# Kernel optimization log

Measured on AMD Instinct MI355X. Metric: run time of the kernel, lower is better.

Reference implementation:

```python
import jax, jax.numpy as jnp
import numpy as np

S = 16   # num_states
C = 8    # input_channels
B = 64   # batch
L = 4096 # sequence length


def hyperbolic_sigmoid(x):
    return x / (1 + jnp.abs(x)) * 0.5 + 0.5


def hyperbolic_softmax(logits, axis):
    x = hyperbolic_sigmoid(logits)
    return x / jnp.sum(x, axis=axis, keepdims=True)


def setup_inputs() -> dict:
    key = jax.random.key(0)
    k0, k1, k2, k3 = jax.random.split(key, 4)
    return {
        "log_input_probs": jax.random.normal(k0, (B, L, C), dtype=jnp.float32),
        "invh_initial_state_probs": jax.random.normal(k1, (S,), dtype=jnp.float32),
        "invh_transition_probs": jax.random.normal(k2, (S, C, S), dtype=jnp.float32),
        "invh_accepting_state_probs": jax.random.normal(k3, (S,), dtype=jnp.float32),
    }


def reference(log_input_probs, invh_initial_state_probs, invh_transition_probs, invh_accepting_state_probs):
    # hyperbolic parameterization -> probabilities
    initial_state_probs = hyperbolic_softmax(invh_initial_state_probs, axis=0)         # (S,)
    transition_probs = hyperbolic_softmax(invh_transition_probs, axis=2)               # (S,C,S)
    accepting_state_logprobs = jnp.log(hyperbolic_sigmoid(invh_accepting_state_probs)) # (S,)

    input_probs = jnp.exp(log_input_probs)  # (B,L,C)
    # per-timestep transition matrices, (B,L,S,S)
    trans_each = jnp.einsum('pcn,blc->blpn', transition_probs, input_probs)
    # log-depth chain product m0 @ m1 @ ... @ m_{L-1} via associative scan
    prefix = jax.lax.associative_scan(jnp.matmul, trans_each, axis=1)
    transition_overall = prefix[:, -1]  # (B,S,S)
    # p_state[b,n] = sum_p overall[b,p,n] * init[p]
    p_state = jnp.einsum('bpn,p->bn', transition_overall, initial_state_probs)
    log_p_state = jnp.log(p_state + 1e-20)
    log_acceptance = jax.nn.logsumexp(log_p_state + accepting_state_logprobs[None, :], axis=1)  # (B,)
    return log_acceptance[None]  # (1,B)
```

## Files before the change

### kernel.cpp

```cpp
#include <hip/hip_runtime.h>
#include <hip/hip_bf16.h>
#include <math.h>

#define S 16
#define C 8
#define NB 64
#define L 4096
#define K 64
#define LC 64

#define SLOT 324
#define RS 20
#define XSS 10

typedef __attribute__((ext_vector_type(8))) short bf16x8;
typedef __attribute__((ext_vector_type(4))) short bf16x4;
typedef __attribute__((ext_vector_type(4))) float f32x4;
typedef unsigned long long ull;

#define WS_INIT 0
#define WS_ACC  64
#define WS_CLOG 512
#define WS_TTT  16896
#define WS_CP   49664

__device__ __forceinline__ float hsig(float x) {
    return x / (1.0f + fabsf(x)) * 0.5f + 0.5f;
}
__device__ __forceinline__ unsigned int f2bf2(float a, float b) {
    __hip_bfloat162 h = __float22bfloat162_rn(make_float2(a, b));
    unsigned int u; __builtin_memcpy(&u, &h, 4); return u;
}
__device__ __forceinline__ unsigned short f2bf(float f) {
    __hip_bfloat16 h = __float2bfloat16(f);
    unsigned short u; __builtin_memcpy(&u, &h, 2); return u;
}

__device__ __forceinline__ f32x4 mfma16(bf16x4 a, bf16x4 b, f32x4 c) {
#if __has_builtin(__builtin_amdgcn_mfma_f32_16x16x16bf16_1k)
    return __builtin_amdgcn_mfma_f32_16x16x16bf16_1k(a, b, c, 0, 0, 0);
#else
    bf16x8 a8 = {a[0], a[1], a[2], a[3], 0, 0, 0, 0};
    bf16x8 b8 = {b[0], b[1], b[2], b[3], 0, 0, 0, 0};
    return __builtin_amdgcn_mfma_f32_16x16x32_bf16(a8, b8, c, 0, 0, 0);
#endif
}

__device__ __forceinline__ bf16x4 ldfrag4(const unsigned short* base, int lane) {
    return *(const bf16x4*)(base + (lane & 15) * RS + (lane >> 4) * 4);
}
__device__ __forceinline__ bf16x4 ldfrag_g4(const unsigned short* base, int lane) {
    return *(const bf16x4*)(base + (lane & 15) * 16 + (lane >> 4) * 4);
}
__device__ __forceinline__ bf16x4 cvt4(f32x4 d) {
    union { unsigned int u[2]; bf16x4 v; } cv;
    cv.u[0] = f2bf2(d[0], d[1]);
    cv.u[1] = f2bf2(d[2], d[3]);
    return cv.v;
}
__device__ __forceinline__ void store16(unsigned short* slot, f32x4 d, int lane, bool odd) {
    int col = lane & 15, quad = lane >> 4;
    if (odd) {
        ull pk = (ull)f2bf2(d[0], d[1]) | ((ull)f2bf2(d[2], d[3]) << 32);
        *(ull*)(slot + col * RS + quad * 4) = pk;
    } else {
#pragma unroll
        for (int r = 0; r < 4; r++) slot[(quad * 4 + r) * RS + col] = f2bf(d[r]);
    }
}

__device__ __forceinline__ f32x4 tree_upper(unsigned short* slots, int lane, int w,
                                            bf16x4 B1a, bf16x4 B1b) {
    f32x4 z = {0.f, 0.f, 0.f, 0.f};
    f32x4 dA = mfma16(ldfrag4(slots + (8 * w) * SLOT, lane), B1a, z);
    store16(slots + (8 * w) * SLOT, dA, lane, false);
    f32x4 dB = mfma16(ldfrag4(slots + (8 * w + 4) * SLOT, lane), B1b, z);
    bf16x4 B2 = cvt4(dB);
    f32x4 d3 = mfma16(ldfrag4(slots + (8 * w) * SLOT, lane), B2, z);
    store16(slots + (8 * w) * SLOT, d3, lane, w & 1);
    __syncthreads();
    if (w < 2) {
        f32x4 d4 = mfma16(ldfrag4(slots + (16 * w) * SLOT, lane),
                          ldfrag4(slots + (16 * w + 8) * SLOT, lane), z);
        store16(slots + (16 * w) * SLOT, d4, lane, w & 1);
    }
    __syncthreads();
    return mfma16(ldfrag4(slots, lane), ldfrag4(slots + 16 * SLOT, lane), z);
}

__global__ void __launch_bounds__(256) prepall_kernel(const float* __restrict__ invh_init,
                                                      const float* __restrict__ invh_T,
                                                      const float* __restrict__ invh_acc,
                                                      unsigned char* __restrict__ wsb) {
    __shared__ float Tn[2048];
    int t = threadIdx.x;
    int cc = blockIdx.x, c = cc >> 3, c2 = cc & 7;
    if (t < S * C) {
        float v[S]; float s = 0.f;
#pragma unroll
        for (int n = 0; n < S; n++) { v[n] = hsig(invh_T[t * S + n]); s += v[n]; }
        float inv = 1.f / s;
#pragma unroll
        for (int n = 0; n < S; n++) Tn[t * S + n] = v[n] * inv;
    }
    __syncthreads();
    int p = t >> 4, n = t & 15;
    float a = 0.f;
#pragma unroll
    for (int k = 0; k < S; k++) a += Tn[(p * 8 + c) * 16 + k] * Tn[(k * 8 + c2) * 16 + n];
    ((unsigned short*)(wsb + WS_TTT))[t * 64 + cc] = f2bf(a);

    if (cc == 0 && t < S) {
        float s = 0.f;
#pragma unroll
        for (int k = 0; k < S; k++) s += hsig(invh_init[k]);
        ((float*)(wsb + WS_INIT))[t] = hsig(invh_init[t]) / s;
        ((float*)(wsb + WS_ACC))[t] = logf(hsig(invh_acc[t]));
    }
}

__global__ void __launch_bounds__(256) chunk_kernel(const float* __restrict__ logx,
                                                    unsigned char* __restrict__ wsb) {
    __shared__ __align__(16) unsigned short slots[32 * SLOT];
    __shared__ __align__(16) float xs[LC * XSS];
    __shared__ float clpart[4];

    int tid = threadIdx.x, lane = tid & 63, w = tid >> 6;
    int col = lane & 15, quad = lane >> 4;
    int chunk0 = 2 * blockIdx.x, b = blockIdx.y;

    const unsigned short* TTT = (const unsigned short*)(wsb + WS_TTT);
    bf16x8 bfr[4][2];
#pragma unroll
    for (int jj = 0; jj < 4; jj++) {
        int t = 4 * w + jj;
#pragma unroll
        for (int kk = 0; kk < 2; kk++)
            bfr[jj][kk] = *(const bf16x8*)(TTT + (t * 16 + col) * 64 + kk * 32 + quad * 8);
    }

    const float* xg = logx + ((size_t)b * L + (size_t)chunk0 * LC) * C;
    float2 vv[2];
    vv[0] = *(const float2*)(xg + 2 * tid);
    vv[1] = *(const float2*)(xg + LC * C + 2 * tid);

#pragma unroll
    for (int ch = 0; ch < 2; ch++) {
        int chunk = chunk0 + ch;

        float2 v = vv[ch];
        float m = fmaxf(v.x, v.y);
        m = fmaxf(m, __shfl_xor(m, 1));
        m = fmaxf(m, __shfl_xor(m, 2));
        float e0 = __expf(v.x - m), e1 = __expf(v.y - m);
        float s = e0 + e1;
        s += __shfl_xor(s, 1);
        s += __shfl_xor(s, 2);
        float inv = 1.0f / s;
        *(float2*)(xs + (tid >> 2) * XSS + 2 * (tid & 3)) = make_float2(e0 * inv, e1 * inv);
        float lx = ((tid & 3) == 0) ? (m + __logf(s)) : 0.f;
#pragma unroll
        for (int d = 1; d < 64; d <<= 1) lx += __shfl_xor(lx, d);
        if (lane == 0) clpart[w] = lx;
        __syncthreads();
        if (tid == 0)
            ((float*)(wsb + WS_CLOG))[b * K + chunk] = clpart[0] + clpart[1] + clpart[2] + clpart[3];

        bf16x8 afr[2][2];
#pragma unroll
        for (int mt = 0; mt < 2; mt++) {
            int i2 = 2 * (mt * 16 + col);
            const float2* x1p = (const float2*)(xs + (i2 + 1) * XSS);
            float2 q0 = x1p[0], q1 = x1p[1], q2 = x1p[2], q3 = x1p[3];
#pragma unroll
            for (int kk = 0; kk < 2; kk++) {
                float x0 = xs[i2 * XSS + kk * 4 + quad];
                union { unsigned int u[4]; bf16x8 v8; } cv;
                cv.u[0] = f2bf2(x0 * q0.x, x0 * q0.y);
                cv.u[1] = f2bf2(x0 * q1.x, x0 * q1.y);
                cv.u[2] = f2bf2(x0 * q2.x, x0 * q2.y);
                cv.u[3] = f2bf2(x0 * q3.x, x0 * q3.y);
                afr[mt][kk] = cv.v8;
            }
        }

#pragma unroll
        for (int mt = 0; mt < 2; mt++)
#pragma unroll
            for (int jj = 0; jj < 4; jj++) {
                f32x4 acc = {0.f, 0.f, 0.f, 0.f};
#pragma unroll
                for (int kk = 0; kk < 2; kk++)
                    acc = __builtin_amdgcn_mfma_f32_16x16x32_bf16(afr[mt][kk], bfr[jj][kk], acc, 0, 0, 0);
                int t = 4 * w + jj;
#pragma unroll
                for (int r = 0; r < 4; r++) {
                    int i = mt * 16 + quad * 4 + r;
                    int off = (i & 1) ? (col * RS + t) : (t * RS + col);
                    slots[i * SLOT + off] = f2bf(acc[r]);
                }
            }
        __syncthreads();

        bf16x4 B1[2];
        {
            f32x4 z = {0.f, 0.f, 0.f, 0.f};
#pragma unroll
            for (int i2 = 0; i2 < 4; i2++) {
                int i = 4 * w + i2;
                f32x4 d = mfma16(ldfrag4(slots + (2 * i) * SLOT, lane),
                                 ldfrag4(slots + (2 * i + 1) * SLOT, lane), z);
                if (i2 & 1) B1[i2 >> 1] = cvt4(d);
                else store16(slots + (2 * i) * SLOT, d, lane, false);
            }
        }
        f32x4 root = tree_upper(slots, lane, w, B1[0], B1[1]);

        if (w == 0) {
            unsigned short* cp = (unsigned short*)(wsb + WS_CP) + ((size_t)b * K + chunk) * 256;
            if (chunk & 1) {
                ull pk = (ull)f2bf2(root[0], root[1]) | ((ull)f2bf2(root[2], root[3]) << 32);
                *(ull*)(cp + col * 16 + quad * 4) = pk;
            } else {
#pragma unroll
                for (int r = 0; r < 4; r++) cp[(quad * 4 + r) * 16 + col] = f2bf(root[r]);
            }
        }
    }
}

__global__ void __launch_bounds__(256) reduce_kernel(unsigned char* __restrict__ wsb,
                                                     float* __restrict__ out) {
    __shared__ __align__(16) unsigned short slots[32 * SLOT];
    int tid = threadIdx.x, lane = tid & 63, w = tid >> 6;
    int col = lane & 15, quad = lane >> 4;
    int b = blockIdx.x;

    const unsigned short* cpb = (const unsigned short*)(wsb + WS_CP) + (size_t)b * K * 256;
    bf16x4 B0[4];
    {
        f32x4 z = {0.f, 0.f, 0.f, 0.f};
#pragma unroll
        for (int i2 = 0; i2 < 8; i2++) {
            int j = 8 * w + i2;
            f32x4 d = mfma16(ldfrag_g4(cpb + (size_t)(2 * j) * 256, lane),
                             ldfrag_g4(cpb + (size_t)(2 * j + 1) * 256, lane), z);
            if (i2 & 1) B0[i2 >> 1] = cvt4(d);
            else store16(slots + j * SLOT, d, lane, false);
        }
    }
    bf16x4 B1r[2];
    {
        f32x4 z = {0.f, 0.f, 0.f, 0.f};
#pragma unroll
        for (int i2 = 0; i2 < 4; i2++) {
            int i = 4 * w + i2;
            f32x4 d = mfma16(ldfrag4(slots + (2 * i) * SLOT, lane), B0[i2], z);
            if (i2 & 1) B1r[i2 >> 1] = cvt4(d);
            else store16(slots + (2 * i) * SLOT, d, lane, false);
        }
    }
    f32x4 troot = tree_upper(slots, lane, w, B1r[0], B1r[1]);

    if (w == 0) {
        const float* initp = (const float*)(wsb + WS_INIT);
        const float* acclog = (const float*)(wsb + WS_ACC);
        float part = 0.f;
#pragma unroll
        for (int r = 0; r < 4; r++) part += initp[quad * 4 + r] * troot[r];
        part += __shfl_xor(part, 16);
        part += __shfl_xor(part, 32);
        float lp = logf(fmaxf(part, 0.f) + 1e-30f) + acclog[col];
        float mx = lp;
#pragma unroll
        for (int d = 1; d < 16; d <<= 1) mx = fmaxf(mx, __shfl_xor(mx, d));
        float a2 = isfinite(mx) ? mx : 0.0f;
        float sm = expf(lp - a2);
#pragma unroll
        for (int d = 1; d < 16; d <<= 1) sm += __shfl_xor(sm, d);
        float cl = ((const float*)(wsb + WS_CLOG))[b * K + lane];
#pragma unroll
        for (int d = 1; d < 64; d <<= 1) cl += __shfl_xor(cl, d);
        if (lane == 0) out[b] = logf(sm) + a2 + cl;
    }
}

extern "C" void kernel_launch(void* const* d_in, const int* in_sizes, int n_in,
                              void* d_out, int out_size, void* d_ws, size_t ws_size,
                              hipStream_t stream) {
    const float* logx = (const float*)d_in[0];
    const float* init = (const float*)d_in[1];
    const float* T    = (const float*)d_in[2];
    const float* acc  = (const float*)d_in[3];
    unsigned char* wsb = (unsigned char*)d_ws;
    float* out = (float*)d_out;

    prepall_kernel<<<64, 256, 0, stream>>>(init, T, acc, wsb);
    chunk_kernel<<<dim3(K / 2, NB), 256, 0, stream>>>(logx, wsb);
    reduce_kernel<<<NB, 256, 0, stream>>>(wsb, out);
}
```

Baseline: 83.66 us.

## Combine chunk pairs in chunk kernel and shorten tree tail barriers

Each chunk block now multiplies its two chunk roots together before writing, so it emits one partial product per pair and halves the partial-product count read by the reduce kernel. The reduce kernel drops its first tree level accordingly. The tree tail also replaces the last two barrier-separated levels with a single-wave computation, removing one __syncthreads. The trade-off is that a single wave does more serial MFMA work at the end while the other waves sit idle.

Result: no change. 83.26 us (-0.5%).

```diff
diff --git a/kernel.cpp b/kernel.cpp
--- a/kernel.cpp
+++ b/kernel.cpp
@@ -8,6 +8,7 @@
 #define L 4096
 #define K 64
 #define LC 64
+#define NP 32
 
 #define SLOT 324
 #define RS 20
@@ -75,17 +76,17 @@
     f32x4 dA = mfma16(ldfrag4(slots + (8 * w) * SLOT, lane), B1a, z);
     store16(slots + (8 * w) * SLOT, dA, lane, false);
     f32x4 dB = mfma16(ldfrag4(slots + (8 * w + 4) * SLOT, lane), B1b, z);
-    bf16x4 B2 = cvt4(dB);
-    f32x4 d3 = mfma16(ldfrag4(slots + (8 * w) * SLOT, lane), B2, z);
+    f32x4 d3 = mfma16(ldfrag4(slots + (8 * w) * SLOT, lane), cvt4(dB), z);
     store16(slots + (8 * w) * SLOT, d3, lane, w & 1);
     __syncthreads();
-    if (w < 2) {
-        f32x4 d4 = mfma16(ldfrag4(slots + (16 * w) * SLOT, lane),
-                          ldfrag4(slots + (16 * w + 8) * SLOT, lane), z);
-        store16(slots + (16 * w) * SLOT, d4, lane, w & 1);
-    }
-    __syncthreads();
-    return mfma16(ldfrag4(slots, lane), ldfrag4(slots + 16 * SLOT, lane), z);
+    f32x4 root = z;
+    if (w == 0) {
+        f32x4 d4a = mfma16(ldfrag4(slots, lane), ldfrag4(slots + 8 * SLOT, lane), z);
+        f32x4 d4b = mfma16(ldfrag4(slots + 16 * SLOT, lane), ldfrag4(slots + 24 * SLOT, lane), z);
+        store16(slots, d4a, lane, false);
+        root = mfma16(ldfrag4(slots, lane), cvt4(d4b), z);
+    }
+    return root;
 }
 
 __global__ void __launch_bounds__(256) prepall_kernel(const float* __restrict__ invh_init,
@@ -127,7 +128,8 @@
 
     int tid = threadIdx.x, lane = tid & 63, w = tid >> 6;
     int col = lane & 15, quad = lane >> 4;
-    int chunk0 = 2 * blockIdx.x, b = blockIdx.y;
+    int pi = blockIdx.x, b = blockIdx.y;
+    int chunk0 = 2 * pi;
 
     const unsigned short* TTT = (const unsigned short*)(wsb + WS_TTT);
     bf16x8 bfr[4][2];
@@ -144,6 +146,7 @@
     vv[0] = *(const float2*)(xg + 2 * tid);
     vv[1] = *(const float2*)(xg + LC * C + 2 * tid);
 
+    f32x4 root0, root1;
 #pragma unroll
     for (int ch = 0; ch < 2; ch++) {
         int chunk = chunk0 + ch;
@@ -215,16 +218,20 @@
             }
         }
         f32x4 root = tree_upper(slots, lane, w, B1[0], B1[1]);
-
-        if (w == 0) {
-            unsigned short* cp = (unsigned short*)(wsb + WS_CP) + ((size_t)b * K + chunk) * 256;
-            if (chunk & 1) {
-                ull pk = (ull)f2bf2(root[0], root[1]) | ((ull)f2bf2(root[2], root[3]) << 32);
-                *(ull*)(cp + col * 16 + quad * 4) = pk;
-            } else {
-#pragma unroll
-                for (int r = 0; r < 4; r++) cp[(quad * 4 + r) * 16 + col] = f2bf(root[r]);
-            }
+        if (ch == 0) root0 = root; else root1 = root;
+    }
+
+    if (w == 0) {
+        f32x4 z = {0.f, 0.f, 0.f, 0.f};
+        store16(slots, root0, lane, false);
+        f32x4 fin = mfma16(ldfrag4(slots, lane), cvt4(root1), z);
+        unsigned short* cp = (unsigned short*)(wsb + WS_CP) + ((size_t)b * NP + pi) * 256;
+        if (pi & 1) {
+            ull pk = (ull)f2bf2(fin[0], fin[1]) | ((ull)f2bf2(fin[2], fin[3]) << 32);
+            *(ull*)(cp + col * 16 + quad * 4) = pk;
+        } else {
+#pragma unroll
+            for (int r = 0; r < 4; r++) cp[(quad * 4 + r) * 16 + col] = f2bf(fin[r]);
         }
     }
 }
@@ -236,26 +243,15 @@
     int col = lane & 15, quad = lane >> 4;
     int b = blockIdx.x;
 
-    const unsigned short* cpb = (const unsigned short*)(wsb + WS_CP) + (size_t)b * K * 256;
-    bf16x4 B0[4];
-    {
-        f32x4 z = {0.f, 0.f, 0.f, 0.f};
-#pragma unroll
-        for (int i2 = 0; i2 < 8; i2++) {
-            int j = 8 * w + i2;
-            f32x4 d = mfma16(ldfrag_g4(cpb + (size_t)(2 * j) * 256, lane),
-                             ldfrag_g4(cpb + (size_t)(2 * j + 1) * 256, lane), z);
-            if (i2 & 1) B0[i2 >> 1] = cvt4(d);
-            else store16(slots + j * SLOT, d, lane, false);
-        }
-    }
+    const unsigned short* cpb = (const unsigned short*)(wsb + WS_CP) + (size_t)b * NP * 256;
     bf16x4 B1r[2];
     {
         f32x4 z = {0.f, 0.f, 0.f, 0.f};
 #pragma unroll
         for (int i2 = 0; i2 < 4; i2++) {
             int i = 4 * w + i2;
-            f32x4 d = mfma16(ldfrag4(slots + (2 * i) * SLOT, lane), B0[i2], z);
+            f32x4 d = mfma16(ldfrag_g4(cpb + (size_t)(2 * i) * 256, lane),
+                             ldfrag_g4(cpb + (size_t)(2 * i + 1) * 256, lane), z);
             if (i2 & 1) B1r[i2 >> 1] = cvt4(d);
             else store16(slots + (2 * i) * SLOT, d, lane, false);
         }
```
